# Kernel optimization log

Hardware: AMD Instinct MI355X
Metric: run time of the kernel (lower is better)

## Reference

```python
import jax, jax.numpy as jnp
import numpy as np

N = 100000       # num_nodes
E = 800000       # num edges (avg degree 8)
EMB = 64         # emb_dim
HID = 256        # hidden_dim


def setup_inputs() -> dict:
    key = jax.random.key(0)
    k1, k2, k3, k4, k5, k6, k7 = jax.random.split(key, 7)
    def xavier(k, fan_in, fan_out):
        limit = float(np.sqrt(6.0 / (fan_in + fan_out)))
        return jax.random.uniform(k, (fan_in, fan_out), jnp.float32, -limit, limit)
    return {
        "row": jax.random.randint(k1, (E,), 0, N, dtype=jnp.int64) if jax.config.jax_enable_x64 else jax.random.randint(k1, (E,), 0, N).astype(jnp.int32),
        "col": jax.random.randint(k2, (E,), 0, N).astype(jnp.int32),
        "val": jax.random.uniform(k3, (E,), jnp.float32),
        "emb": jax.random.normal(k4, (N, EMB), jnp.float32) * 0.02,
        "W0": xavier(k5, EMB, HID),
        "W1": xavier(k6, HID, HID),
        "W2": xavier(k7, HID, HID),
    }


def reference(row, col, val, emb, W0, W1, W2):
    # SpMM: out[r] = sum_{edges e with row[e]==r} val[e] * emb[col[e]]
    msgs = val[:, None] * emb[col]                      # [E, EMB] gather + scale
    x = jax.ops.segment_sum(msgs, row, num_segments=N)  # [N, EMB] scatter-add
    # MLP (bias-free linears; dropout=0.0 / eval mode => identity)
    x = jax.nn.relu(x @ W0)   # [N, HID]
    x = jax.nn.relu(x @ W1)   # [N, HID]
    x = x @ W2                # [N, HID]
    return x
```

## Files before the change

kernel.cpp:

```cpp
#include <hip/hip_runtime.h>
#include <hip/hip_bf16.h>

#define EMB 64
#define HID 256

typedef __attribute__((ext_vector_type(8))) short short8_t;
typedef __attribute__((ext_vector_type(4))) float f32x4;

__device__ __forceinline__ unsigned short f2bf(float f)
{
    union { float f; unsigned int u; } c; c.f = f;
    unsigned int u = c.u;
    u += 0x7fffu + ((u >> 16) & 1u);
    return (unsigned short)(u >> 16);
}
__device__ __forceinline__ float bf2f(unsigned short b)
{
    union { unsigned int u; float f; } c; c.u = ((unsigned int)b) << 16;
    return c.f;
}

__global__ __launch_bounds__(256) void prep_kernel(
    const float* __restrict__ emb, const float* __restrict__ W0,
    const float* __restrict__ W1, const float* __restrict__ W2,
    int* __restrict__ counts, unsigned short* __restrict__ embb,
    unsigned short* __restrict__ W0f, unsigned short* __restrict__ W1f,
    unsigned short* __restrict__ W2f, int M, int zb, int cb)
{
    int b = blockIdx.x;
    if (b < zb) {
        int idx = (b * 256 + threadIdx.x) * 4;
        if (idx + 3 < M) {
            int4 z; z.x = 0; z.y = 0; z.z = 0; z.w = 0;
            *(int4*)&counts[idx] = z;
        } else {
            for (int i = idx; i < M; ++i) counts[i] = 0;
        }
        return;
    }
    b -= zb;
    if (b < cb) {
        int idx = (b * 256 + threadIdx.x) * 4;
        if (idx + 3 < M * EMB) {
            float4 v = *(const float4*)&emb[idx];
            ushort4 o;
            o.x = f2bf(v.x); o.y = f2bf(v.y); o.z = f2bf(v.z); o.w = f2bf(v.w);
            *(ushort4*)&embb[idx] = o;
        }
        return;
    }
    b -= cb;
    if (b < 8) {
        int i    = b * 256 + threadIdx.x;
        int lane = i & 63;
        int kc   = (i >> 6) & 1;
        int nt   = i >> 7;
        int lr   = lane & 15, kg = lane >> 4;
        unsigned short tmp[8];
#pragma unroll
        for (int j = 0; j < 8; ++j)
            tmp[j] = f2bf(W0[(kc * 32 + kg * 8 + j) * HID + nt * 16 + lr]);
        *(short8_t*)&W0f[(size_t)i * 8] = *(short8_t*)tmp;
        return;
    }
    b -= 8;
    if (b < 32) {
        int i    = b * 256 + threadIdx.x;
        int lane = i & 63;
        int kc   = (i >> 6) & 7;
        int nt   = i >> 9;
        int lr   = lane & 15, kg = lane >> 4;
        unsigned short tmp[8];
#pragma unroll
        for (int j = 0; j < 8; ++j)
            tmp[j] = f2bf(W1[(kc * 32 + kg * 8 + j) * HID + nt * 16 + lr]);
        *(short8_t*)&W1f[(size_t)i * 8] = *(short8_t*)tmp;
        return;
    }
    b -= 32;
    {
        int i    = b * 256 + threadIdx.x;
        int lane = i & 63;
        int kc   = (i >> 6) & 7;
        int nt   = i >> 9;
        int lr   = lane & 15, kg = lane >> 4;
        unsigned short tmp[8];
#pragma unroll
        for (int j = 0; j < 8; ++j)
            tmp[j] = f2bf(W2[(kc * 32 + kg * 8 + j) * HID + nt * 16 + lr]);
        *(short8_t*)&W2f[(size_t)i * 8] = *(short8_t*)tmp;
    }
}

__global__ __launch_bounds__(256) void hist_kernel(
    const int* __restrict__ row, int* __restrict__ counts, int E)
{
    int base = (blockIdx.x * 256 + threadIdx.x) * 4;
    if (base + 3 < E) {
        int4 r4 = *(const int4*)&row[base];
        atomicAdd(&counts[r4.x], 1);
        atomicAdd(&counts[r4.y], 1);
        atomicAdd(&counts[r4.z], 1);
        atomicAdd(&counts[r4.w], 1);
    } else {
        for (int i = base; i < E; ++i) atomicAdd(&counts[row[i]], 1);
    }
}

__global__ __launch_bounds__(256) void scan_phase1(
    const int* __restrict__ counts, int* __restrict__ excl,
    int* __restrict__ blockSums, int n)
{
    __shared__ int s[256];
    int t = threadIdx.x;
    int base = blockIdx.x * 1024 + t * 4;
    int4 v = {0, 0, 0, 0};
    if (base + 3 < n) {
        v = *(const int4*)&counts[base];
    } else {
        if (base + 0 < n) v.x = counts[base + 0];
        if (base + 1 < n) v.y = counts[base + 1];
        if (base + 2 < n) v.z = counts[base + 2];
        if (base + 3 < n) v.w = counts[base + 3];
    }
    int tsum = v.x + v.y + v.z + v.w;
    s[t] = tsum;
    __syncthreads();
#pragma unroll
    for (int off = 1; off < 256; off <<= 1) {
        int val = (t >= off) ? s[t - off] : 0;
        __syncthreads();
        s[t] += val;
        __syncthreads();
    }
    if (t == 255) blockSums[blockIdx.x] = s[255];
    int e0 = s[t] - tsum;
    int e1 = e0 + v.x;
    int e2 = e1 + v.y;
    int e3 = e2 + v.z;
    if (base + 0 < n) excl[base + 0] = e0;
    if (base + 1 < n) excl[base + 1] = e1;
    if (base + 2 < n) excl[base + 2] = e2;
    if (base + 3 < n) excl[base + 3] = e3;
}

__global__ __launch_bounds__(256) void scan_phase2(int* blockSums, int nb)
{
    __shared__ int s[256];
    int t = threadIdx.x;
    int v = (t < nb) ? blockSums[t] : 0;
    s[t] = v;
    __syncthreads();
#pragma unroll
    for (int off = 1; off < 256; off <<= 1) {
        int val = (t >= off) ? s[t - off] : 0;
        __syncthreads();
        s[t] += val;
        __syncthreads();
    }
    if (t < nb) blockSums[t] = s[t] - v;
}

__global__ __launch_bounds__(256) void scan_phase3(
    int* __restrict__ offsets, const int* __restrict__ blockSums,
    int* __restrict__ cursor, int n)
{
    int i = blockIdx.x * 256 + threadIdx.x;
    if (i >= n) return;
    int o = offsets[i] + blockSums[i >> 10];
    offsets[i] = o;
    cursor[i]  = o;
}

__global__ __launch_bounds__(256) void scatter_kernel(
    const int* __restrict__ row, const int* __restrict__ col,
    const float* __restrict__ val, int* __restrict__ cursor,
    uint2* __restrict__ edata, int E)
{
    int e = blockIdx.x * 256 + threadIdx.x;
    if (e >= E) return;
    int r = row[e];
    int pos = atomicAdd(&cursor[r], 1);
    uint2 d;
    d.x = (unsigned)col[e];
    d.y = __float_as_uint(val[e]);
    edata[pos] = d;
}

#define ROWS_PER_WAVE 8
__global__ __launch_bounds__(256) void pull_kernel(
    const int* __restrict__ offsets, const int* __restrict__ counts,
    const uint2* __restrict__ edata, const unsigned short* __restrict__ embb,
    unsigned short* __restrict__ xb, int Nn)
{
    const int nw   = gridDim.x * 4;
    const int wid  = blockIdx.x * 4 + (threadIdx.x >> 6);
    const int lane = threadIdx.x & 63;
    if (wid >= Nn) return;

    int beg = __builtin_amdgcn_readfirstlane(offsets[wid]);
    int cnt = __builtin_amdgcn_readfirstlane(counts[wid]);
    for (int r = wid; r < Nn; r += nw) {
        int rn = r + nw;
        int begN = 0, cntN = 0;
        if (rn < Nn) {
            begN = __builtin_amdgcn_readfirstlane(offsets[rn]);
            cntN = __builtin_amdgcn_readfirstlane(counts[rn]);
        }

        float acc = 0.f;
        for (int i = 0; i < cnt; i += 8) {
            uint2 ed[8];
#pragma unroll
            for (int j = 0; j < 8; ++j) {
                int idx = i + j;
                idx = (idx < cnt) ? idx : (cnt - 1);
                ed[j] = edata[beg + idx];
            }
            float g[8];
#pragma unroll
            for (int j = 0; j < 8; ++j)
                g[j] = bf2f(embb[(size_t)ed[j].x * EMB + lane]);
#pragma unroll
            for (int j = 0; j < 8; ++j) {
                float v = (i + j < cnt) ? __uint_as_float(ed[j].y) : 0.f;
                acc += v * g[j];
            }
        }
        xb[(size_t)r * EMB + lane] = f2bf(acc);
        beg = begN; cnt = cntN;
    }
}

__global__ __launch_bounds__(256) void mlp_fused(
    const unsigned short* __restrict__ xb,
    const unsigned short* __restrict__ W0f,
    const unsigned short* __restrict__ W1f,
    const unsigned short* __restrict__ W2f,
    float* __restrict__ out, int M)
{
    __shared__ unsigned short H[32 * 256];

    const int t    = threadIdx.x;
    const int lane = t & 63;
    const int w    = t >> 6;
    const int lr   = lane & 15;
    const int kg   = lane >> 4;
    const int row0 = blockIdx.x * 32;
    char* Hb = (char*)H;

#define HOFF(row, bytecol) ((((row) * 512) + (bytecol)) ^ (((row) & 7) << 4))

    short8_t ax[2][2];
#pragma unroll
    for (int kc = 0; kc < 2; ++kc)
#pragma unroll
        for (int m = 0; m < 2; ++m) {
            int gr = row0 + m * 16 + lr;
            ax[kc][m] = *(const short8_t*)(xb + (size_t)(gr < M ? gr : 0) * EMB
                                           + kc * 32 + kg * 8);
        }
    f32x4 acc[2][4] = {};
#pragma unroll
    for (int kc = 0; kc < 2; ++kc) {
        short8_t b[4];
#pragma unroll
        for (int n = 0; n < 4; ++n)
            b[n] = *(const short8_t*)&W0f[(size_t)(((w * 4 + n) * 2 + kc) * 64 + lane) * 8];
#pragma unroll
        for (int m = 0; m < 2; ++m)
#pragma unroll
            for (int n = 0; n < 4; ++n)
                acc[m][n] = __builtin_amdgcn_mfma_f32_16x16x32_bf16(
                    ax[kc][m], b[n], acc[m][n], 0, 0, 0);
    }

    short8_t pb[2][4];
#pragma unroll
    for (int n = 0; n < 4; ++n) {
        pb[0][n] = *(const short8_t*)&W1f[(size_t)(((w * 4 + n) * 8 + 0) * 64 + lane) * 8];
        pb[1][n] = *(const short8_t*)&W1f[(size_t)(((w * 4 + n) * 8 + 1) * 64 + lane) * 8];
    }

#pragma unroll
    for (int m = 0; m < 2; ++m)
#pragma unroll
        for (int r = 0; r < 4; ++r)
#pragma unroll
            for (int n = 0; n < 4; ++n)
                *(unsigned short*)(Hb + HOFF(m * 16 + kg * 4 + r,
                                             (w * 64 + n * 16 + lr) * 2)) =
                    f2bf(fmaxf(acc[m][n][r], 0.f));
    __syncthreads();

    f32x4 acc2[2][4] = {};
#pragma unroll
    for (int kc = 0; kc < 8; ++kc) {
        short8_t b[4];
#pragma unroll
        for (int n = 0; n < 4; ++n) b[n] = pb[kc & 1][n];
#pragma unroll
        for (int n = 0; n < 4; ++n) {
            if (kc < 6)
                pb[kc & 1][n] = *(const short8_t*)
                    &W1f[(size_t)(((w * 4 + n) * 8 + kc + 2) * 64 + lane) * 8];
            else
                pb[kc & 1][n] = *(const short8_t*)
                    &W2f[(size_t)(((w * 4 + n) * 8 + (kc - 6)) * 64 + lane) * 8];
        }
        short8_t a[2];
#pragma unroll
        for (int m = 0; m < 2; ++m)
            a[m] = *(const short8_t*)(Hb + HOFF(m * 16 + lr, kc * 64 + kg * 16));
#pragma unroll
        for (int m = 0; m < 2; ++m)
#pragma unroll
            for (int n = 0; n < 4; ++n)
                acc2[m][n] = __builtin_amdgcn_mfma_f32_16x16x32_bf16(
                    a[m], b[n], acc2[m][n], 0, 0, 0);
    }
    __syncthreads();
#pragma unroll
    for (int m = 0; m < 2; ++m)
#pragma unroll
        for (int r = 0; r < 4; ++r)
#pragma unroll
            for (int n = 0; n < 4; ++n)
                *(unsigned short*)(Hb + HOFF(m * 16 + kg * 4 + r,
                                             (w * 64 + n * 16 + lr) * 2)) =
                    f2bf(fmaxf(acc2[m][n][r], 0.f));
    __syncthreads();

    f32x4 acc3[2][4] = {};
#pragma unroll
    for (int kc = 0; kc < 8; ++kc) {
        short8_t b[4];
#pragma unroll
        for (int n = 0; n < 4; ++n) b[n] = pb[kc & 1][n];
#pragma unroll
        for (int n = 0; n < 4; ++n) {
            if (kc < 6)
                pb[kc & 1][n] = *(const short8_t*)
                    &W2f[(size_t)(((w * 4 + n) * 8 + kc + 2) * 64 + lane) * 8];
        }
        short8_t a[2];
#pragma unroll
        for (int m = 0; m < 2; ++m)
            a[m] = *(const short8_t*)(Hb + HOFF(m * 16 + lr, kc * 64 + kg * 16));
#pragma unroll
        for (int m = 0; m < 2; ++m)
#pragma unroll
            for (int n = 0; n < 4; ++n)
                acc3[m][n] = __builtin_amdgcn_mfma_f32_16x16x32_bf16(
                    a[m], b[n], acc3[m][n], 0, 0, 0);
    }
    __syncthreads();

    float* Hf = (float*)H;
#pragma unroll
    for (int m = 0; m < 2; ++m) {
#pragma unroll
        for (int n = 0; n < 4; ++n)
#pragma unroll
            for (int r = 0; r < 4; ++r)
                Hf[w * 1024 + (kg * 4 + r) * 64 + n * 16 + lr] = acc3[m][n][r];
#pragma unroll
        for (int p = 0; p < 4; ++p) {
            int rl = (lane >> 4) + p * 4;
            f32x4 v = *(const f32x4*)&Hf[w * 1024 + rl * 64 + (lane & 15) * 4];
            int gr = row0 + m * 16 + rl;
            if (gr < M)
                *(f32x4*)&out[(size_t)gr * HID + w * 64 + (lane & 15) * 4] = v;
        }
    }
#undef HOFF
}

__global__ __launch_bounds__(256) void spmm_kernel(
    const int* __restrict__ row, const int* __restrict__ col,
    const float* __restrict__ val, const float* __restrict__ emb,
    float* __restrict__ x, int E)
{
    int gid  = blockIdx.x * blockDim.x + threadIdx.x;
    int e    = gid >> 6;
    int lane = gid & 63;
    if (e >= E) return;
    unsafeAtomicAdd(&x[(size_t)row[e] * EMB + lane],
                    val[e] * emb[(size_t)col[e] * EMB + lane]);
}

template<int K, bool RELU>
__global__ __launch_bounds__(256) void gemm_f32(
    const float* A, const float* __restrict__ B, float* C, int M)
{
    __shared__ float As[64][17];
    __shared__ float Bs[16][256];

    const int t    = threadIdx.x;
    const int tn   = t & 15;
    const int row0 = blockIdx.x * 64;
    const int sk = t & 15;
    const int sm = (t >> 4) * 4;

    float acc[4][16];
#pragma unroll
    for (int i = 0; i < 4; ++i)
#pragma unroll
        for (int j = 0; j < 16; ++j) acc[i][j] = 0.f;

    const int mB = ((t & 63) >> 4) * 4;
    const int wq = t >> 6;
    const int myM = (wq * 16) + mB;

    for (int k0 = 0; k0 < K; k0 += 16) {
        __syncthreads();
#pragma unroll
        for (int i = 0; i < 4; ++i) {
            int m  = sm + i;
            int gr = row0 + m;
            As[m][sk] = (gr < M) ? A[(size_t)gr * K + k0 + sk] : 0.f;
        }
#pragma unroll
        for (int r = 0; r < 16; ++r)
            Bs[r][t] = B[(size_t)(k0 + r) * 256 + t];
        __syncthreads();

#pragma unroll
        for (int kk = 0; kk < 16; ++kk) {
            float a0 = As[myM + 0][kk];
            float a1 = As[myM + 1][kk];
            float a2 = As[myM + 2][kk];
            float a3 = As[myM + 3][kk];
            float4 b[4];
#pragma unroll
            for (int j = 0; j < 4; ++j)
                b[j] = *(const float4*)&Bs[kk][tn * 4 + j * 64];
#pragma unroll
            for (int j = 0; j < 4; ++j) {
                acc[0][j*4+0] += a0 * b[j].x;  acc[0][j*4+1] += a0 * b[j].y;
                acc[0][j*4+2] += a0 * b[j].z;  acc[0][j*4+3] += a0 * b[j].w;
                acc[1][j*4+0] += a1 * b[j].x;  acc[1][j*4+1] += a1 * b[j].y;
                acc[1][j*4+2] += a1 * b[j].z;  acc[1][j*4+3] += a1 * b[j].w;
                acc[2][j*4+0] += a2 * b[j].x;  acc[2][j*4+1] += a2 * b[j].y;
                acc[2][j*4+2] += a2 * b[j].z;  acc[2][j*4+3] += a2 * b[j].w;
                acc[3][j*4+0] += a3 * b[j].x;  acc[3][j*4+1] += a3 * b[j].y;
                acc[3][j*4+2] += a3 * b[j].z;  acc[3][j*4+3] += a3 * b[j].w;
            }
        }
    }

#pragma unroll
    for (int i = 0; i < 4; ++i) {
        int gr = row0 + myM + i;
        if (gr < M) {
#pragma unroll
            for (int j = 0; j < 4; ++j) {
                float4 o;
                o.x = acc[i][j*4+0]; o.y = acc[i][j*4+1];
                o.z = acc[i][j*4+2]; o.w = acc[i][j*4+3];
                if (RELU) {
                    o.x = fmaxf(o.x, 0.f); o.y = fmaxf(o.y, 0.f);
                    o.z = fmaxf(o.z, 0.f); o.w = fmaxf(o.w, 0.f);
                }
                *(float4*)&C[(size_t)gr * 256 + tn * 4 + j * 64] = o;
            }
        }
    }
}

extern "C" void kernel_launch(void* const* d_in, const int* in_sizes, int n_in,
                              void* d_out, int out_size, void* d_ws, size_t ws_size,
                              hipStream_t stream)
{
    const int*   row = (const int*)d_in[0];
    const int*   col = (const int*)d_in[1];
    const float* val = (const float*)d_in[2];
    const float* emb = (const float*)d_in[3];
    const float* W0  = (const float*)d_in[4];
    const float* W1  = (const float*)d_in[5];
    const float* W2  = (const float*)d_in[6];
    float* out = (float*)d_out;

    const int E = in_sizes[0];
    const int M = in_sizes[3] / EMB;

    char* ws = (char*)d_ws;

    size_t off = 0;
    auto alloc = [&](size_t bytes) { size_t o = off; off = (off + bytes + 255) & ~(size_t)255; return o; };
    const size_t off_counts = alloc((size_t)M * 4);
    const size_t off_offs   = alloc((size_t)M * 4);
    const size_t off_cursor = alloc((size_t)M * 4);
    const size_t off_bsums  = alloc(1024);
    const size_t off_edata  = alloc((size_t)E * 8);
    const size_t off_embb   = alloc((size_t)M * EMB * 2);
    const size_t off_xb     = alloc((size_t)M * EMB * 2);
    const size_t off_w0     = alloc((size_t)EMB * HID * 2);
    const size_t off_w1     = alloc((size_t)HID * HID * 2);
    const size_t off_w2     = alloc((size_t)HID * HID * 2);
    const size_t need       = off;

    if (ws_size >= need) {
        int*   counts = (int*)(ws + off_counts);
        int*   offs   = (int*)(ws + off_offs);
        int*   cursor = (int*)(ws + off_cursor);
        int*   bsums  = (int*)(ws + off_bsums);
        uint2* edata  = (uint2*)(ws + off_edata);
        unsigned short* embb = (unsigned short*)(ws + off_embb);
        unsigned short* xb  = (unsigned short*)(ws + off_xb);
        unsigned short* W0f = (unsigned short*)(ws + off_w0);
        unsigned short* W1f = (unsigned short*)(ws + off_w1);
        unsigned short* W2f = (unsigned short*)(ws + off_w2);

        int zb = (M / 4 + 255) / 256;
        int cb = ((M * EMB) / 4 + 255) / 256;
        int prep_blocks = zb + cb + 8 + 32 + 32;
        prep_kernel<<<prep_blocks, 256, 0, stream>>>(
            emb, W0, W1, W2, counts, embb, W0f, W1f, W2f, M, zb, cb);

        hist_kernel<<<(E / 4 + 255) / 256, 256, 0, stream>>>(row, counts, E);
        int nb = (M + 1023) / 1024;
        scan_phase1<<<nb, 256, 0, stream>>>(counts, offs, bsums, M);
        scan_phase2<<<1, 256, 0, stream>>>(bsums, nb);
        scan_phase3<<<(M + 255) / 256, 256, 0, stream>>>(offs, bsums, cursor, M);
        scatter_kernel<<<(E + 255) / 256, 256, 0, stream>>>(row, col, val, cursor, edata, E);

        int pull_blocks = (M + 4 * ROWS_PER_WAVE - 1) / (4 * ROWS_PER_WAVE);
        pull_kernel<<<pull_blocks, 256, 0, stream>>>(offs, counts, edata, embb, xb, M);

        int gblocks = (M + 31) / 32;
        mlp_fused<<<gblocks, 256, 0, stream>>>(xb, W0f, W1f, W2f, out, M);
    } else {
        float* x = (float*)ws;
        (void)hipMemsetAsync(x, 0, (size_t)M * EMB * sizeof(float), stream);
        spmm_kernel<<<(E + 3) / 4, 256, 0, stream>>>(row, col, val, emb, x, E);
        int gblocks = (M + 63) / 64;
        gemm_f32<EMB, true ><<<gblocks, 256, 0, stream>>>(x,   W0, out, M);
        gemm_f32<HID, true ><<<gblocks, 256, 0, stream>>>(out, W1, out, M);
        gemm_f32<HID, false><<<gblocks, 256, 0, stream>>>(out, W2, out, M);
    }
}
```

Before: 194.8 us.

## Vectorize SpMM pull gathers across lane groups and fuse scan phases

The pull kernel now splits each wave into four 16-lane groups. Each group handles different edges and loads 4 bf16 values per lane with 8-byte gathers, and the groups are combined by cross-lane shuffle reductions before a packed 8-byte store. This replaces 2-byte per-lane gathers with wider loads and lowers per-edge instruction count. Separately, scan phases 2 and 3 are merged into one kernel in which every block redundantly rescans the block sums, which removes one launch at the cost of duplicated small scans.

```diff
diff --git a/kernel.cpp b/kernel.cpp
--- a/kernel.cpp
+++ b/kernel.cpp
@@ -144,9 +144,12 @@
     if (base + 3 < n) excl[base + 3] = e3;
 }
 
-__global__ __launch_bounds__(256) void scan_phase2(int* blockSums, int nb)
+__global__ __launch_bounds__(256) void scan_phase23(
+    int* __restrict__ offsets, const int* __restrict__ blockSums,
+    int* __restrict__ cursor, int n, int nb)
 {
     __shared__ int s[256];
+    __shared__ int ex[256];
     int t = threadIdx.x;
     int v = (t < nb) ? blockSums[t] : 0;
     s[t] = v;
@@ -158,18 +161,14 @@
         s[t] += val;
         __syncthreads();
     }
-    if (t < nb) blockSums[t] = s[t] - v;
-}
-
-__global__ __launch_bounds__(256) void scan_phase3(
-    int* __restrict__ offsets, const int* __restrict__ blockSums,
-    int* __restrict__ cursor, int n)
-{
-    int i = blockIdx.x * 256 + threadIdx.x;
-    if (i >= n) return;
-    int o = offsets[i] + blockSums[i >> 10];
-    offsets[i] = o;
-    cursor[i]  = o;
+    ex[t] = s[t] - v;
+    __syncthreads();
+    int i = blockIdx.x * 256 + t;
+    if (i < n) {
+        int o = offsets[i] + ex[i >> 10];
+        offsets[i] = o;
+        cursor[i]  = o;
+    }
 }
 
 __global__ __launch_bounds__(256) void scatter_kernel(
@@ -196,6 +195,8 @@
     const int nw   = gridDim.x * 4;
     const int wid  = blockIdx.x * 4 + (threadIdx.x >> 6);
     const int lane = threadIdx.x & 63;
+    const int g    = lane >> 4;
+    const int sl   = lane & 15;
     if (wid >= Nn) return;
 
     int beg = __builtin_amdgcn_readfirstlane(offsets[wid]);
@@ -208,26 +209,39 @@
             cntN = __builtin_amdgcn_readfirstlane(counts[rn]);
         }
 
-        float acc = 0.f;
+        f32x4 acc = {0.f, 0.f, 0.f, 0.f};
         for (int i = 0; i < cnt; i += 8) {
-            uint2 ed[8];
-#pragma unroll
-            for (int j = 0; j < 8; ++j) {
-                int idx = i + j;
-                idx = (idx < cnt) ? idx : (cnt - 1);
-                ed[j] = edata[beg + idx];
-            }
-            float g[8];
-#pragma unroll
-            for (int j = 0; j < 8; ++j)
-                g[j] = bf2f(embb[(size_t)ed[j].x * EMB + lane]);
-#pragma unroll
-            for (int j = 0; j < 8; ++j) {
-                float v = (i + j < cnt) ? __uint_as_float(ed[j].y) : 0.f;
-                acc += v * g[j];
-            }
-        }
-        xb[(size_t)r * EMB + lane] = f2bf(acc);
+            int i0 = i + g;       bool c0 = (i0 < cnt); i0 = c0 ? i0 : 0;
+            int i1 = i + 4 + g;   bool c1 = (i1 < cnt); i1 = c1 ? i1 : 0;
+            uint2 ed0 = edata[beg + i0];
+            uint2 ed1 = edata[beg + i1];
+            uint2 g0 = *(const uint2*)&embb[(size_t)ed0.x * EMB + sl * 4];
+            uint2 g1 = *(const uint2*)&embb[(size_t)ed1.x * EMB + sl * 4];
+            float v0 = c0 ? __uint_as_float(ed0.y) : 0.f;
+            float v1 = c1 ? __uint_as_float(ed1.y) : 0.f;
+            acc.x += v0 * bf2f((unsigned short)(g0.x & 0xffffu));
+            acc.y += v0 * bf2f((unsigned short)(g0.x >> 16));
+            acc.z += v0 * bf2f((unsigned short)(g0.y & 0xffffu));
+            acc.w += v0 * bf2f((unsigned short)(g0.y >> 16));
+            acc.x += v1 * bf2f((unsigned short)(g1.x & 0xffffu));
+            acc.y += v1 * bf2f((unsigned short)(g1.x >> 16));
+            acc.z += v1 * bf2f((unsigned short)(g1.y & 0xffffu));
+            acc.w += v1 * bf2f((unsigned short)(g1.y >> 16));
+        }
+        acc.x += __shfl_xor(acc.x, 16, 64);
+        acc.y += __shfl_xor(acc.y, 16, 64);
+        acc.z += __shfl_xor(acc.z, 16, 64);
+        acc.w += __shfl_xor(acc.w, 16, 64);
+        acc.x += __shfl_xor(acc.x, 32, 64);
+        acc.y += __shfl_xor(acc.y, 32, 64);
+        acc.z += __shfl_xor(acc.z, 32, 64);
+        acc.w += __shfl_xor(acc.w, 32, 64);
+        if (g == 0) {
+            uint2 o;
+            o.x = (unsigned)f2bf(acc.x) | ((unsigned)f2bf(acc.y) << 16);
+            o.y = (unsigned)f2bf(acc.z) | ((unsigned)f2bf(acc.w) << 16);
+            *(uint2*)&xb[(size_t)r * EMB + sl * 4] = o;
+        }
         beg = begN; cnt = cntN;
     }
 }
@@ -521,8 +535,7 @@
         hist_kernel<<<(E / 4 + 255) / 256, 256, 0, stream>>>(row, counts, E);
         int nb = (M + 1023) / 1024;
         scan_phase1<<<nb, 256, 0, stream>>>(counts, offs, bsums, M);
-        scan_phase2<<<1, 256, 0, stream>>>(bsums, nb);
-        scan_phase3<<<(M + 255) / 256, 256, 0, stream>>>(offs, bsums, cursor, M);
+        scan_phase23<<<(M + 255) / 256, 256, 0, stream>>>(offs, bsums, cursor, M, nb);
         scatter_kernel<<<(E + 255) / 256, 256, 0, stream>>>(row, col, val, cursor, edata, E);
 
         int pull_blocks = (M + 4 * ROWS_PER_WAVE - 1) / (4 * ROWS_PER_WAVE);
```

New measurement: 175.9 us (median of 2 runs). -9.7%, faster.
